# Performance work log

Measured on AMD Instinct MI355X. Metric: run time of the kernel, lower is better.

Reference implementation:

```python
import jax, jax.numpy as jnp
import numpy as np

N_HEADS = 16

def setup_inputs() -> dict:
    key = jax.random.key(0)
    qkv = jax.random.normal(key, (8, 3072, 1024), dtype=jnp.float32)
    return {"qkv": qkv}

def reference(qkv) -> jnp.ndarray:
    B, D, L = qkv.shape
    q, k, v = jnp.split(qkv, 3, axis=1)            # each [B, H*ch, L]
    ch = D // (3 * N_HEADS)
    scale = 1.0 / np.sqrt(np.sqrt(ch)).astype(np.float32)
    q = (q * scale).reshape(B * N_HEADS, ch, L)
    k = (k * scale).reshape(B * N_HEADS, ch, L)
    v = v.reshape(B * N_HEADS, ch, L)
    weight = jnp.einsum('bct,bcs->bts', q, k)       # [B*H, L, L]
    weight = jax.nn.softmax(weight, axis=-1)
    z = jnp.einsum('bts,bcs->bct', weight, v)       # [B*H, ch, L]
    return z.reshape(B, -1, L)
```

## Files before the change

kernel.cpp:

```cpp
#include <hip/hip_runtime.h>


typedef __attribute__((ext_vector_type(8))) _Float16 f16x8;
typedef __attribute__((ext_vector_type(4))) _Float16 f16x4;
typedef __attribute__((ext_vector_type(4))) float f32x4;

#define MAT_HALVES 8388608
#define WS_BYTES   33554432

#define ASYNC16(g, l) __builtin_amdgcn_global_load_lds(                    \
    (__attribute__((address_space(1))) void*)(void*)(g),                   \
    (__attribute__((address_space(3))) void*)(void*)(l), 16, 0, 0)

__global__ __launch_bounds__(256) void prepass_kv(
    const float* __restrict__ qkv, _Float16* __restrict__ ws) {
    __shared__ float ft[64][68];
    const int tid = threadIdx.x;
    const int bid = blockIdx.x;
    const int mat = bid >> 11;
    const int idx = bid & 2047;
    const int head = idx >> 4;
    const int blk  = idx & 15;
    const int b = head >> 4, h = head & 15;
    const float* src = qkv + (size_t)b * 3072 * 1024
                           + (size_t)((1 + mat) * 1024 + h * 64) * 1024;
    const int s0 = blk * 64;
    if (mat == 0) {
#pragma unroll
        for (int i = 0; i < 4; ++i) {
            const int c = i * 16 + (tid >> 4);
            const int s = (tid & 15) * 4;
            const float4 v = *(const float4*)(src + (size_t)c * 1024 + s0 + s);
            ft[s + 0][c] = v.x;
            ft[s + 1][c] = v.y;
            ft[s + 2][c] = v.z;
            ft[s + 3][c] = v.w;
        }
        __syncthreads();
        _Float16* dst = ws + (size_t)head * 65536 + (size_t)s0 * 64;
#pragma unroll
        for (int r = 0; r < 2; ++r) {
            const int g = r * 256 + tid;
            const int t = g >> 3, cb = g & 7;
            const float4 a = *(const float4*)&ft[t][cb * 8];
            const float4 bq = *(const float4*)&ft[t][cb * 8 + 4];
            f16x8 o = { (_Float16)a.x,  (_Float16)a.y,  (_Float16)a.z,  (_Float16)a.w,
                        (_Float16)bq.x, (_Float16)bq.y, (_Float16)bq.z, (_Float16)bq.w };
            *(f16x8*)(dst + (size_t)t * 64 + (size_t)(cb ^ (t & 7)) * 8) = o;
        }
    } else {
        _Float16* dst = ws + (size_t)MAT_HALVES + (size_t)head * 65536;
#pragma unroll
        for (int i = 0; i < 4; ++i) {
            const int c = i * 16 + (tid >> 4);
            const int s = (tid & 15) * 4;
            const float4 v = *(const float4*)(src + (size_t)c * 1024 + s0 + s);
            f16x4 o = { (_Float16)v.x, (_Float16)v.y, (_Float16)v.z, (_Float16)v.w };
            const int sb = s >> 3, pos = s & 7;
            *(f16x4*)(dst + (size_t)c * 1024 + s0 + (size_t)((sb ^ (c & 7)) * 8 + pos)) = o;
        }
    }
}

__launch_bounds__(512, 4)
__global__ void attn_kernel(const float* __restrict__ qkv,
                            const _Float16* __restrict__ ws,
                            float* __restrict__ out) {
    __shared__ __align__(16) union SM {
        _Float16 kv[2][8192];
        float ft[64][68];
    } sm;

    const int tid  = threadIdx.x;
    const int wv   = tid >> 6;
    const int lane = tid & 63;
    const int li   = lane & 15;
    const int quad = lane >> 4;

    const int bid  = blockIdx.x;
    const int head = (bid >> 5) * 8 + (bid & 7);
    const int tt   = (bid >> 3) & 3;
    const int t0   = tt * 256;

    const int b = head >> 4, h = head & 15;
    const float* qsrc = qkv + (size_t)b * 3072 * 1024 + (size_t)(h * 64) * 1024;
    const _Float16* kt = ws + (size_t)head * 65536;
    const _Float16* vh = ws + (size_t)MAT_HALVES + (size_t)head * 65536;

    const float qscale = 0.125f * 1.44269504f;
    f16x8 bqf[2][2];
    {
        const int ci = tid >> 4;
        const int tq = (tid & 15) * 4;
        for (int ct = 0; ct < 4; ++ct) {
#pragma unroll
            for (int i = 0; i < 2; ++i) {
                const int c = i * 32 + ci;
                const float4 v = *(const float4*)(qsrc + (size_t)c * 1024 + t0 + ct * 64 + tq);
                sm.ft[tq + 0][c] = v.x * qscale;
                sm.ft[tq + 1][c] = v.y * qscale;
                sm.ft[tq + 2][c] = v.z * qscale;
                sm.ft[tq + 3][c] = v.w * qscale;
            }
            __syncthreads();
            if ((wv >> 1) == ct) {
#pragma unroll
                for (int sub = 0; sub < 2; ++sub) {
                    const int tl = (wv & 1) * 32 + sub * 16 + li;
#pragma unroll
                    for (int kk = 0; kk < 2; ++kk) {
                        const int c0 = (kk * 4 + quad) * 8;
                        const float4 a  = *(const float4*)&sm.ft[tl][c0];
                        const float4 b2 = *(const float4*)&sm.ft[tl][c0 + 4];
                        bqf[sub][kk] = f16x8{ (_Float16)a.x,  (_Float16)a.y,
                                              (_Float16)a.z,  (_Float16)a.w,
                                              (_Float16)b2.x, (_Float16)b2.y,
                                              (_Float16)b2.z, (_Float16)b2.w };
                    }
                }
            }
            __syncthreads();
        }
    }

    ASYNC16(kt + (size_t)tid * 8, &sm.kv[0][tid * 8]);
    ASYNC16(vh + (size_t)(tid >> 3) * 1024 + (size_t)(tid & 7) * 8,
            &sm.kv[0][4096 + tid * 8]);

    f32x4 accz[2][4] = {};
    float psum[2] = {};

    for (int si = 0; si < 16; ++si) {
        __syncthreads();
        if (si < 15) {
            const int s0n = (si + 1) * 64;
            const int nb = (si + 1) & 1;
            ASYNC16(kt + (size_t)s0n * 64 + (size_t)tid * 8, &sm.kv[nb][tid * 8]);
            ASYNC16(vh + (size_t)(tid >> 3) * 1024 + s0n + (size_t)(tid & 7) * 8,
                    &sm.kv[nb][4096 + tid * 8]);
        }
        const _Float16* Kl = &sm.kv[si & 1][0];
        const _Float16* Vl = &sm.kv[si & 1][4096];

#pragma unroll
        for (int ns = 0; ns < 4; ++ns) {
            f16x8 ak[2];
#pragma unroll
            for (int kk = 0; kk < 2; ++kk) {
                const int cb = (kk * 4 + quad) ^ (li & 7);
                ak[kk] = *(const f16x8*)&Kl[(ns * 16 + li) * 64 + cb * 8];
            }
            f16x4 pk[2];
#pragma unroll
            for (int sub = 0; sub < 2; ++sub) {
                f32x4 st = {};
                st = __builtin_amdgcn_mfma_f32_16x16x32_f16(ak[0], bqf[sub][0], st, 0, 0, 0);
                st = __builtin_amdgcn_mfma_f32_16x16x32_f16(ak[1], bqf[sub][1], st, 0, 0, 0);
                const float p0 = __builtin_amdgcn_exp2f(st[0]);
                const float p1 = __builtin_amdgcn_exp2f(st[1]);
                const float p2 = __builtin_amdgcn_exp2f(st[2]);
                const float p3 = __builtin_amdgcn_exp2f(st[3]);
                psum[sub] += (p0 + p1) + (p2 + p3);
                pk[sub] = f16x4{ (_Float16)p0, (_Float16)p1,
                                 (_Float16)p2, (_Float16)p3 };
            }
            const int sb  = 2 * ns + (quad >> 1);
            const int pos = (quad & 1) * 4;
#pragma unroll
            for (int nc = 0; nc < 4; ++nc) {
                const int c = nc * 16 + li;
                f16x4 bv = *(const f16x4*)&Vl[c * 64 + ((sb ^ (c & 7)) << 3) + pos];
                accz[0][nc] = __builtin_amdgcn_mfma_f32_16x16x16f16(
                    pk[0], bv, accz[0][nc], 0, 0, 0);
                accz[1][nc] = __builtin_amdgcn_mfma_f32_16x16x16f16(
                    pk[1], bv, accz[1][nc], 0, 0, 0);
            }
        }
    }

    float rl[2][4];
#pragma unroll
    for (int sub = 0; sub < 2; ++sub) {
        float s = psum[sub];
        s += __shfl_xor(s, 16);
        s += __shfl_xor(s, 32);
#pragma unroll
        for (int r = 0; r < 4; ++r)
            rl[sub][r] = 1.0f / __shfl(s, quad * 4 + r);
    }

    float* obase = out + (size_t)b * 1024 * 1024
                       + (size_t)(h * 64) * 1024 + t0;
#pragma unroll
    for (int sub = 0; sub < 2; ++sub)
#pragma unroll
        for (int nc = 0; nc < 4; ++nc) {
            const int c = nc * 16 + li;
            const int t = wv * 32 + sub * 16 + quad * 4;
            f32x4 z = accz[sub][nc];
            float4 o = { z[0] * rl[sub][0], z[1] * rl[sub][1],
                         z[2] * rl[sub][2], z[3] * rl[sub][3] };
            *(float4*)(obase + (size_t)c * 1024 + t) = o;
        }
}

struct S1fb {
    _Float16 K[64][72];
    _Float16 V[64][72];
    _Float16 P[128][72];
};
union SMemFb {
    S1fb s1;
    float zt[64][132];
};

__launch_bounds__(256, 4)
__global__ void qkv_attn_fallback(const float* __restrict__ qkv,
                                  float* __restrict__ out) {
    constexpr int L = 1024;
    __shared__ SMemFb sm;
    const int tid  = threadIdx.x;
    const int wv   = tid >> 6;
    const int lane = tid & 63;
    const int li   = lane & 15;
    const int quad = lane >> 4;
    const int bid  = blockIdx.x;
    const int head = (bid >> 6) * 8 + (bid & 7);
    const int tt   = (bid >> 3) & 7;
    const int b = head >> 4;
    const int h = head & 15;
    const float* qbase = qkv + (size_t)b * 3072 * L + (size_t)(h * 64) * L;
    const float* kbase = qbase + (size_t)1024 * L;
    const float* vbase = qbase + (size_t)2048 * L;
    float*       obase = out + (size_t)b * 1024 * L + (size_t)(h * 64) * L;
    const int t0 = tt * 128;
#pragma unroll
    for (int i = 0; i < 4; ++i) {
        const int c = i * 16 + (tid >> 4);
        const int t = (tid & 15) * 8;
        const float4 qa = *(const float4*)(qbase + (size_t)c * L + t0 + t);
        const float4 qb = *(const float4*)(qbase + (size_t)c * L + t0 + t + 4);
        sm.s1.P[t + 0][c] = (_Float16)(qa.x * 0.125f);
        sm.s1.P[t + 1][c] = (_Float16)(qa.y * 0.125f);
        sm.s1.P[t + 2][c] = (_Float16)(qa.z * 0.125f);
        sm.s1.P[t + 3][c] = (_Float16)(qa.w * 0.125f);
        sm.s1.P[t + 4][c] = (_Float16)(qb.x * 0.125f);
        sm.s1.P[t + 5][c] = (_Float16)(qb.y * 0.125f);
        sm.s1.P[t + 6][c] = (_Float16)(qb.z * 0.125f);
        sm.s1.P[t + 7][c] = (_Float16)(qb.w * 0.125f);
    }
    __syncthreads();
    f16x8 aq0[2], aq1[2];
#pragma unroll
    for (int kk = 0; kk < 2; ++kk) {
        aq0[kk] = *(const f16x8*)&sm.s1.P[wv * 32 + li][kk * 32 + quad * 8];
        aq1[kk] = *(const f16x8*)&sm.s1.P[wv * 32 + 16 + li][kk * 32 + quad * 8];
    }
    f32x4 accz0[4] = {}, accz1[4] = {};
    float psum0[4] = {}, psum1[4] = {};
    float4 kreg[4], vreg[4];
#pragma unroll
    for (int i = 0; i < 4; ++i) {
        const int c = i * 16 + (tid >> 4);
        const int s = (tid & 15) * 4;
        kreg[i] = *(const float4*)(kbase + (size_t)c * L + s);
        vreg[i] = *(const float4*)(vbase + (size_t)c * L + s);
    }
    for (int si = 0; si < 16; ++si) {
        __syncthreads();
#pragma unroll
        for (int i = 0; i < 4; ++i) {
            const int c = i * 16 + (tid >> 4);
            const int s = (tid & 15) * 4;
            sm.s1.K[s + 0][c] = (_Float16)kreg[i].x;
            sm.s1.K[s + 1][c] = (_Float16)kreg[i].y;
            sm.s1.K[s + 2][c] = (_Float16)kreg[i].z;
            sm.s1.K[s + 3][c] = (_Float16)kreg[i].w;
            f16x4 pv = { (_Float16)vreg[i].x, (_Float16)vreg[i].y,
                         (_Float16)vreg[i].z, (_Float16)vreg[i].w };
            *(f16x4*)&sm.s1.V[c][s] = pv;
        }
        __syncthreads();
        if (si < 15) {
            const int s0n = (si + 1) * 64;
#pragma unroll
            for (int i = 0; i < 4; ++i) {
                const int c = i * 16 + (tid >> 4);
                const int s = (tid & 15) * 4;
                kreg[i] = *(const float4*)(kbase + (size_t)c * L + s0n + s);
                vreg[i] = *(const float4*)(vbase + (size_t)c * L + s0n + s);
            }
        }
#pragma unroll
        for (int nt = 0; nt < 4; ++nt) {
            f32x4 a0 = {}, a1 = {};
#pragma unroll
            for (int kk = 0; kk < 2; ++kk) {
                f16x8 bk = *(const f16x8*)&sm.s1.K[nt * 16 + li][kk * 32 + quad * 8];
                a0 = __builtin_amdgcn_mfma_f32_16x16x32_f16(aq0[kk], bk, a0, 0, 0, 0);
                a1 = __builtin_amdgcn_mfma_f32_16x16x32_f16(aq1[kk], bk, a1, 0, 0, 0);
            }
#pragma unroll
            for (int r = 0; r < 4; ++r) {
                const float p0 = __expf(a0[r]);
                const float p1 = __expf(a1[r]);
                psum0[r] += p0;
                psum1[r] += p1;
                sm.s1.P[wv * 32 + quad * 4 + r][nt * 16 + li] = (_Float16)p0;
                sm.s1.P[wv * 32 + 16 + quad * 4 + r][nt * 16 + li] = (_Float16)p1;
            }
        }
#pragma unroll
        for (int kk = 0; kk < 2; ++kk) {
            f16x8 ap0 = *(const f16x8*)&sm.s1.P[wv * 32 + li][kk * 32 + quad * 8];
            f16x8 ap1 = *(const f16x8*)&sm.s1.P[wv * 32 + 16 + li][kk * 32 + quad * 8];
#pragma unroll
            for (int nt = 0; nt < 4; ++nt) {
                f16x8 bv = *(const f16x8*)&sm.s1.V[nt * 16 + li][kk * 32 + quad * 8];
                accz0[nt] = __builtin_amdgcn_mfma_f32_16x16x32_f16(ap0, bv, accz0[nt], 0, 0, 0);
                accz1[nt] = __builtin_amdgcn_mfma_f32_16x16x32_f16(ap1, bv, accz1[nt], 0, 0, 0);
            }
        }
    }
    float rl0[4], rl1[4];
#pragma unroll
    for (int r = 0; r < 4; ++r) {
        float s0 = psum0[r], s1 = psum1[r];
        s0 += __shfl_xor(s0, 1); s0 += __shfl_xor(s0, 2);
        s0 += __shfl_xor(s0, 4); s0 += __shfl_xor(s0, 8);
        s1 += __shfl_xor(s1, 1); s1 += __shfl_xor(s1, 2);
        s1 += __shfl_xor(s1, 4); s1 += __shfl_xor(s1, 8);
        rl0[r] = 1.0f / s0;
        rl1[r] = 1.0f / s1;
    }
    __syncthreads();
#pragma unroll
    for (int nt = 0; nt < 4; ++nt)
#pragma unroll
        for (int r = 0; r < 4; ++r) {
            sm.zt[nt * 16 + li][wv * 32 + quad * 4 + r]      = accz0[nt][r] * rl0[r];
            sm.zt[nt * 16 + li][wv * 32 + 16 + quad * 4 + r] = accz1[nt][r] * rl1[r];
        }
    __syncthreads();
#pragma unroll
    for (int i = 0; i < 8; ++i) {
        const int c = i * 8 + (tid >> 5);
        const int t = (tid & 31) * 4;
        float4 o = { sm.zt[c][t], sm.zt[c][t + 1],
                     sm.zt[c][t + 2], sm.zt[c][t + 3] };
        *(float4*)(obase + (size_t)c * L + t0 + t) = o;
    }
}

extern "C" void kernel_launch(void* const* d_in, const int* in_sizes, int n_in,
                              void* d_out, int out_size, void* d_ws, size_t ws_size,
                              hipStream_t stream) {
    const float* qkv = (const float*)d_in[0];
    float* out = (float*)d_out;
    if (ws_size >= (size_t)WS_BYTES) {
        _Float16* ws = (_Float16*)d_ws;
        prepass_kv<<<4096, 256, 0, stream>>>(qkv, ws);
        attn_kernel<<<512, 512, 0, stream>>>(qkv, ws, out);
    } else {
        qkv_attn_fallback<<<1024, 256, 0, stream>>>(qkv, out);
    }
}
```

Baseline: 195.9 us.

## Deepen K/V LDS pipeline to four buffers and overlap prologue loads with Q staging

Grows the K/V shared-memory ring from two to four 16KB stages. The first two tiles are prefetched before Q is processed, and each barrier step now covers two tiles, which halves the number of __syncthreads in the main loop. All Q global loads are also hoisted into registers before the LDS transpose, so their latencies overlap. The cost is 64KB of LDS per block instead of 32KB plus more live registers, which may reduce how many blocks fit on each CU.

```diff
diff --git a/kernel.cpp b/kernel.cpp
--- a/kernel.cpp
+++ b/kernel.cpp
@@ -67,7 +67,7 @@
                             const _Float16* __restrict__ ws,
                             float* __restrict__ out) {
     __shared__ __align__(16) union SM {
-        _Float16 kv[2][8192];
+        _Float16 kv[4][8192];
         float ft[64][68];
     } sm;
 
@@ -87,93 +87,111 @@
     const _Float16* kt = ws + (size_t)head * 65536;
     const _Float16* vh = ws + (size_t)MAT_HALVES + (size_t)head * 65536;
 
+#pragma unroll
+    for (int u = 0; u < 2; ++u) {
+        const int s0 = u * 64;
+        ASYNC16(kt + (size_t)s0 * 64 + (size_t)tid * 8, &sm.kv[2 + u][tid * 8]);
+        ASYNC16(vh + (size_t)(tid >> 3) * 1024 + s0 + (size_t)(tid & 7) * 8,
+                &sm.kv[2 + u][4096 + tid * 8]);
+    }
+
     const float qscale = 0.125f * 1.44269504f;
+    const int ci = tid >> 4;
+    const int tq = (tid & 15) * 4;
+    float4 qv[4][2];
+#pragma unroll
+    for (int ct = 0; ct < 4; ++ct)
+#pragma unroll
+        for (int i = 0; i < 2; ++i) {
+            const int c = i * 32 + ci;
+            qv[ct][i] = *(const float4*)(qsrc + (size_t)c * 1024 + t0 + ct * 64 + tq);
+        }
     f16x8 bqf[2][2];
-    {
-        const int ci = tid >> 4;
-        const int tq = (tid & 15) * 4;
-        for (int ct = 0; ct < 4; ++ct) {
-#pragma unroll
-            for (int i = 0; i < 2; ++i) {
-                const int c = i * 32 + ci;
-                const float4 v = *(const float4*)(qsrc + (size_t)c * 1024 + t0 + ct * 64 + tq);
-                sm.ft[tq + 0][c] = v.x * qscale;
-                sm.ft[tq + 1][c] = v.y * qscale;
-                sm.ft[tq + 2][c] = v.z * qscale;
-                sm.ft[tq + 3][c] = v.w * qscale;
-            }
-            __syncthreads();
-            if ((wv >> 1) == ct) {
-#pragma unroll
-                for (int sub = 0; sub < 2; ++sub) {
-                    const int tl = (wv & 1) * 32 + sub * 16 + li;
-#pragma unroll
-                    for (int kk = 0; kk < 2; ++kk) {
-                        const int c0 = (kk * 4 + quad) * 8;
-                        const float4 a  = *(const float4*)&sm.ft[tl][c0];
-                        const float4 b2 = *(const float4*)&sm.ft[tl][c0 + 4];
-                        bqf[sub][kk] = f16x8{ (_Float16)a.x,  (_Float16)a.y,
-                                              (_Float16)a.z,  (_Float16)a.w,
-                                              (_Float16)b2.x, (_Float16)b2.y,
-                                              (_Float16)b2.z, (_Float16)b2.w };
-                    }
+#pragma unroll
+    for (int ct = 0; ct < 4; ++ct) {
+#pragma unroll
+        for (int i = 0; i < 2; ++i) {
+            const int c = i * 32 + ci;
+            sm.ft[tq + 0][c] = qv[ct][i].x * qscale;
+            sm.ft[tq + 1][c] = qv[ct][i].y * qscale;
+            sm.ft[tq + 2][c] = qv[ct][i].z * qscale;
+            sm.ft[tq + 3][c] = qv[ct][i].w * qscale;
+        }
+        __syncthreads();
+        if ((wv >> 1) == ct) {
+#pragma unroll
+            for (int sub = 0; sub < 2; ++sub) {
+                const int tl = (wv & 1) * 32 + sub * 16 + li;
+#pragma unroll
+                for (int kk = 0; kk < 2; ++kk) {
+                    const int c0 = (kk * 4 + quad) * 8;
+                    const float4 a  = *(const float4*)&sm.ft[tl][c0];
+                    const float4 b2 = *(const float4*)&sm.ft[tl][c0 + 4];
+                    bqf[sub][kk] = f16x8{ (_Float16)a.x,  (_Float16)a.y,
+                                          (_Float16)a.z,  (_Float16)a.w,
+                                          (_Float16)b2.x, (_Float16)b2.y,
+                                          (_Float16)b2.z, (_Float16)b2.w };
                 }
             }
-            __syncthreads();
-        }
-    }
-
-    ASYNC16(kt + (size_t)tid * 8, &sm.kv[0][tid * 8]);
-    ASYNC16(vh + (size_t)(tid >> 3) * 1024 + (size_t)(tid & 7) * 8,
-            &sm.kv[0][4096 + tid * 8]);
+        }
+        __syncthreads();
+    }
 
     f32x4 accz[2][4] = {};
     float psum[2] = {};
 
-    for (int si = 0; si < 16; ++si) {
-        __syncthreads();
-        if (si < 15) {
-            const int s0n = (si + 1) * 64;
-            const int nb = (si + 1) & 1;
-            ASYNC16(kt + (size_t)s0n * 64 + (size_t)tid * 8, &sm.kv[nb][tid * 8]);
-            ASYNC16(vh + (size_t)(tid >> 3) * 1024 + s0n + (size_t)(tid & 7) * 8,
-                    &sm.kv[nb][4096 + tid * 8]);
-        }
-        const _Float16* Kl = &sm.kv[si & 1][0];
-        const _Float16* Vl = &sm.kv[si & 1][4096];
-
-#pragma unroll
-        for (int ns = 0; ns < 4; ++ns) {
-            f16x8 ak[2];
-#pragma unroll
-            for (int kk = 0; kk < 2; ++kk) {
-                const int cb = (kk * 4 + quad) ^ (li & 7);
-                ak[kk] = *(const f16x8*)&Kl[(ns * 16 + li) * 64 + cb * 8];
-            }
-            f16x4 pk[2];
-#pragma unroll
-            for (int sub = 0; sub < 2; ++sub) {
-                f32x4 st = {};
-                st = __builtin_amdgcn_mfma_f32_16x16x32_f16(ak[0], bqf[sub][0], st, 0, 0, 0);
-                st = __builtin_amdgcn_mfma_f32_16x16x32_f16(ak[1], bqf[sub][1], st, 0, 0, 0);
-                const float p0 = __builtin_amdgcn_exp2f(st[0]);
-                const float p1 = __builtin_amdgcn_exp2f(st[1]);
-                const float p2 = __builtin_amdgcn_exp2f(st[2]);
-                const float p3 = __builtin_amdgcn_exp2f(st[3]);
-                psum[sub] += (p0 + p1) + (p2 + p3);
-                pk[sub] = f16x4{ (_Float16)p0, (_Float16)p1,
-                                 (_Float16)p2, (_Float16)p3 };
-            }
-            const int sb  = 2 * ns + (quad >> 1);
-            const int pos = (quad & 1) * 4;
-#pragma unroll
-            for (int nc = 0; nc < 4; ++nc) {
-                const int c = nc * 16 + li;
-                f16x4 bv = *(const f16x4*)&Vl[c * 64 + ((sb ^ (c & 7)) << 3) + pos];
-                accz[0][nc] = __builtin_amdgcn_mfma_f32_16x16x16f16(
-                    pk[0], bv, accz[0][nc], 0, 0, 0);
-                accz[1][nc] = __builtin_amdgcn_mfma_f32_16x16x16f16(
-                    pk[1], bv, accz[1][nc], 0, 0, 0);
+    for (int p = 0; p < 8; ++p) {
+        __syncthreads();
+        if (p < 7) {
+#pragma unroll
+            for (int u = 0; u < 2; ++u) {
+                const int sn  = 2 * p + 2 + u;
+                const int s0n = sn * 64;
+                const int nb  = (sn + 2) & 3;
+                ASYNC16(kt + (size_t)s0n * 64 + (size_t)tid * 8, &sm.kv[nb][tid * 8]);
+                ASYNC16(vh + (size_t)(tid >> 3) * 1024 + s0n + (size_t)(tid & 7) * 8,
+                        &sm.kv[nb][4096 + tid * 8]);
+            }
+        }
+#pragma unroll
+        for (int u = 0; u < 2; ++u) {
+            const int si = 2 * p + u;
+            const _Float16* Kl = &sm.kv[(si + 2) & 3][0];
+            const _Float16* Vl = &sm.kv[(si + 2) & 3][4096];
+
+#pragma unroll
+            for (int ns = 0; ns < 4; ++ns) {
+                f16x8 ak[2];
+#pragma unroll
+                for (int kk = 0; kk < 2; ++kk) {
+                    const int cb = (kk * 4 + quad) ^ (li & 7);
+                    ak[kk] = *(const f16x8*)&Kl[(ns * 16 + li) * 64 + cb * 8];
+                }
+                f16x4 pk[2];
+#pragma unroll
+                for (int sub = 0; sub < 2; ++sub) {
+                    f32x4 st = {};
+                    st = __builtin_amdgcn_mfma_f32_16x16x32_f16(ak[0], bqf[sub][0], st, 0, 0, 0);
+                    st = __builtin_amdgcn_mfma_f32_16x16x32_f16(ak[1], bqf[sub][1], st, 0, 0, 0);
+                    const float p0 = __builtin_amdgcn_exp2f(st[0]);
+                    const float p1 = __builtin_amdgcn_exp2f(st[1]);
+                    const float p2 = __builtin_amdgcn_exp2f(st[2]);
+                    const float p3 = __builtin_amdgcn_exp2f(st[3]);
+                    psum[sub] += (p0 + p1) + (p2 + p3);
+                    pk[sub] = f16x4{ (_Float16)p0, (_Float16)p1,
+                                     (_Float16)p2, (_Float16)p3 };
+                }
+                const int sb  = 2 * ns + (quad >> 1);
+                const int pos = (quad & 1) * 4;
+#pragma unroll
+                for (int nc = 0; nc < 4; ++nc) {
+                    const int c = nc * 16 + li;
+                    f16x4 bv = *(const f16x4*)&Vl[c * 64 + ((sb ^ (c & 7)) << 3) + pos];
+                    accz[0][nc] = __builtin_amdgcn_mfma_f32_16x16x16f16(
+                        pk[0], bv, accz[0][nc], 0, 0, 0);
+                    accz[1][nc] = __builtin_amdgcn_mfma_f32_16x16x16f16(
+                        pk[1], bv, accz[1][nc], 0, 0, 0);
+                }
             }
         }
     }
```

Measured after the change: 229.9 us. +17.4%, slower.

## Halve attention block to 4 waves, each computing 64 query rows

Applied to the files above, without the earlier changes.

The attention kernel now launches 256 threads instead of 512. Each wave processes 64 query rows (4 sub-tiles) instead of 32, so every K/V fragment read from LDS feeds twice as many MFMAs. The K/V shared buffers are no longer unioned with the Q transpose buffer, which lets the first two K/V tiles be prefetched asynchronously before the Q load. s_setprio is raised around the MFMA loop. The cost is more accumulator registers per thread and fewer waves per block to hide latency, with occupancy bounded at 2 blocks.

```diff
diff --git a/kernel.cpp b/kernel.cpp
--- a/kernel.cpp
+++ b/kernel.cpp
@@ -62,14 +62,12 @@
     }
 }
 
-__launch_bounds__(512, 4)
+__launch_bounds__(256, 2)
 __global__ void attn_kernel(const float* __restrict__ qkv,
                             const _Float16* __restrict__ ws,
                             float* __restrict__ out) {
-    __shared__ __align__(16) union SM {
-        _Float16 kv[2][8192];
-        float ft[64][68];
-    } sm;
+    __shared__ __align__(16) _Float16 kv[2][8192];
+    __shared__ __align__(16) float ft[64][68];
 
     const int tid  = threadIdx.x;
     const int wv   = tid >> 6;
@@ -87,61 +85,71 @@
     const _Float16* kt = ws + (size_t)head * 65536;
     const _Float16* vh = ws + (size_t)MAT_HALVES + (size_t)head * 65536;
 
+#pragma unroll
+    for (int u = 0; u < 2; ++u) {
+        const int s0 = u * 64;
+#pragma unroll
+        for (int j = 0; j < 2; ++j) {
+            const int g = j * 256 + tid;
+            ASYNC16(kt + (size_t)s0 * 64 + (size_t)g * 8, &kv[u][g * 8]);
+            ASYNC16(vh + (size_t)(g >> 3) * 1024 + s0 + (size_t)(g & 7) * 8,
+                    &kv[u][4096 + g * 8]);
+        }
+    }
+
     const float qscale = 0.125f * 1.44269504f;
-    f16x8 bqf[2][2];
-    {
-        const int ci = tid >> 4;
-        const int tq = (tid & 15) * 4;
-        for (int ct = 0; ct < 4; ++ct) {
-#pragma unroll
-            for (int i = 0; i < 2; ++i) {
-                const int c = i * 32 + ci;
-                const float4 v = *(const float4*)(qsrc + (size_t)c * 1024 + t0 + ct * 64 + tq);
-                sm.ft[tq + 0][c] = v.x * qscale;
-                sm.ft[tq + 1][c] = v.y * qscale;
-                sm.ft[tq + 2][c] = v.z * qscale;
-                sm.ft[tq + 3][c] = v.w * qscale;
-            }
-            __syncthreads();
-            if ((wv >> 1) == ct) {
-#pragma unroll
-                for (int sub = 0; sub < 2; ++sub) {
-                    const int tl = (wv & 1) * 32 + sub * 16 + li;
-#pragma unroll
-                    for (int kk = 0; kk < 2; ++kk) {
-                        const int c0 = (kk * 4 + quad) * 8;
-                        const float4 a  = *(const float4*)&sm.ft[tl][c0];
-                        const float4 b2 = *(const float4*)&sm.ft[tl][c0 + 4];
-                        bqf[sub][kk] = f16x8{ (_Float16)a.x,  (_Float16)a.y,
-                                              (_Float16)a.z,  (_Float16)a.w,
-                                              (_Float16)b2.x, (_Float16)b2.y,
-                                              (_Float16)b2.z, (_Float16)b2.w };
-                    }
+    f16x8 bqf[4][2];
+    for (int ct = 0; ct < 4; ++ct) {
+#pragma unroll
+        for (int i = 0; i < 4; ++i) {
+            const int c = i * 16 + (tid >> 4);
+            const int t = (tid & 15) * 4;
+            const float4 v = *(const float4*)(qsrc + (size_t)c * 1024 + t0 + ct * 64 + t);
+            ft[t + 0][c] = v.x * qscale;
+            ft[t + 1][c] = v.y * qscale;
+            ft[t + 2][c] = v.z * qscale;
+            ft[t + 3][c] = v.w * qscale;
+        }
+        __syncthreads();
+        if (wv == ct) {
+#pragma unroll
+            for (int sub = 0; sub < 4; ++sub) {
+                const int tl = sub * 16 + li;
+#pragma unroll
+                for (int kk = 0; kk < 2; ++kk) {
+                    const int c0 = (kk * 4 + quad) * 8;
+                    const float4 a  = *(const float4*)&ft[tl][c0];
+                    const float4 b2 = *(const float4*)&ft[tl][c0 + 4];
+                    bqf[sub][kk] = f16x8{ (_Float16)a.x,  (_Float16)a.y,
+                                          (_Float16)a.z,  (_Float16)a.w,
+                                          (_Float16)b2.x, (_Float16)b2.y,
+                                          (_Float16)b2.z, (_Float16)b2.w };
                 }
             }
-            __syncthreads();
-        }
-    }
-
-    ASYNC16(kt + (size_t)tid * 8, &sm.kv[0][tid * 8]);
-    ASYNC16(vh + (size_t)(tid >> 3) * 1024 + (size_t)(tid & 7) * 8,
-            &sm.kv[0][4096 + tid * 8]);
-
-    f32x4 accz[2][4] = {};
-    float psum[2] = {};
+        }
+        __syncthreads();
+    }
+
+    f32x4 accz[4][4] = {};
+    float psum[4] = {};
 
     for (int si = 0; si < 16; ++si) {
         __syncthreads();
         if (si < 15) {
             const int s0n = (si + 1) * 64;
             const int nb = (si + 1) & 1;
-            ASYNC16(kt + (size_t)s0n * 64 + (size_t)tid * 8, &sm.kv[nb][tid * 8]);
-            ASYNC16(vh + (size_t)(tid >> 3) * 1024 + s0n + (size_t)(tid & 7) * 8,
-                    &sm.kv[nb][4096 + tid * 8]);
-        }
-        const _Float16* Kl = &sm.kv[si & 1][0];
-        const _Float16* Vl = &sm.kv[si & 1][4096];
-
+#pragma unroll
+            for (int j = 0; j < 2; ++j) {
+                const int g = j * 256 + tid;
+                ASYNC16(kt + (size_t)s0n * 64 + (size_t)g * 8, &kv[nb][g * 8]);
+                ASYNC16(vh + (size_t)(g >> 3) * 1024 + s0n + (size_t)(g & 7) * 8,
+                        &kv[nb][4096 + g * 8]);
+            }
+        }
+        const _Float16* Kl = &kv[si & 1][0];
+        const _Float16* Vl = &kv[si & 1][4096];
+
+        __builtin_amdgcn_s_setprio(1);
 #pragma unroll
         for (int ns = 0; ns < 4; ++ns) {
             f16x8 ak[2];
@@ -150,9 +158,9 @@
                 const int cb = (kk * 4 + quad) ^ (li & 7);
                 ak[kk] = *(const f16x8*)&Kl[(ns * 16 + li) * 64 + cb * 8];
             }
-            f16x4 pk[2];
-#pragma unroll
-            for (int sub = 0; sub < 2; ++sub) {
+            f16x4 pk[4];
+#pragma unroll
+            for (int sub = 0; sub < 4; ++sub) {
                 f32x4 st = {};
                 st = __builtin_amdgcn_mfma_f32_16x16x32_f16(ak[0], bqf[sub][0], st, 0, 0, 0);
                 st = __builtin_amdgcn_mfma_f32_16x16x32_f16(ak[1], bqf[sub][1], st, 0, 0, 0);
@@ -170,17 +178,18 @@
             for (int nc = 0; nc < 4; ++nc) {
                 const int c = nc * 16 + li;
                 f16x4 bv = *(const f16x4*)&Vl[c * 64 + ((sb ^ (c & 7)) << 3) + pos];
-                accz[0][nc] = __builtin_amdgcn_mfma_f32_16x16x16f16(
-                    pk[0], bv, accz[0][nc], 0, 0, 0);
-                accz[1][nc] = __builtin_amdgcn_mfma_f32_16x16x16f16(
-                    pk[1], bv, accz[1][nc], 0, 0, 0);
-            }
-        }
-    }
-
-    float rl[2][4];
-#pragma unroll
-    for (int sub = 0; sub < 2; ++sub) {
+#pragma unroll
+                for (int sub = 0; sub < 4; ++sub)
+                    accz[sub][nc] = __builtin_amdgcn_mfma_f32_16x16x16f16(
+                        pk[sub], bv, accz[sub][nc], 0, 0, 0);
+            }
+        }
+        __builtin_amdgcn_s_setprio(0);
+    }
+
+    float rl[4][4];
+#pragma unroll
+    for (int sub = 0; sub < 4; ++sub) {
         float s = psum[sub];
         s += __shfl_xor(s, 16);
         s += __shfl_xor(s, 32);
@@ -192,11 +201,11 @@
     float* obase = out + (size_t)b * 1024 * 1024
                        + (size_t)(h * 64) * 1024 + t0;
 #pragma unroll
-    for (int sub = 0; sub < 2; ++sub)
+    for (int sub = 0; sub < 4; ++sub)
 #pragma unroll
         for (int nc = 0; nc < 4; ++nc) {
             const int c = nc * 16 + li;
-            const int t = wv * 32 + sub * 16 + quad * 4;
+            const int t = wv * 64 + sub * 16 + quad * 4;
             f32x4 z = accz[sub][nc];
             float4 o = { z[0] * rl[sub][0], z[1] * rl[sub][1],
                          z[2] * rl[sub][2], z[3] * rl[sub][3] };
@@ -360,7 +369,7 @@
     if (ws_size >= (size_t)WS_BYTES) {
         _Float16* ws = (_Float16*)d_ws;
         prepass_kv<<<4096, 256, 0, stream>>>(qkv, ws);
-        attn_kernel<<<512, 512, 0, stream>>>(qkv, ws, out);
+        attn_kernel<<<512, 256, 0, stream>>>(qkv, ws, out);
     } else {
         qkv_attn_fallback<<<1024, 256, 0, stream>>>(qkv, out);
     }
```

Result: no change. 193.3 us (-1.3%).

## Load V directly from global into registers and prefetch K before Q setup

Applied to the files above, without the earlier changes.

V tiles are no longer staged through double-buffered LDS. Each thread loads its MFMA B-operand fragments of V straight from global memory into registers at the start of each step, and the prepass stops swizzling V. K's first two tiles are prefetched asynchronously before the Q transpose, which now uses its own LDS buffer instead of a union, and setprio is raised around the MFMA loop. The occupancy hint drops from 4 to 2. This saves LDS traffic and space for V and overlaps the K load with Q setup, at the cost of strided, less coalesced global loads of V and more register pressure.

```diff
diff --git a/kernel.cpp b/kernel.cpp
--- a/kernel.cpp
+++ b/kernel.cpp
@@ -56,20 +56,17 @@
             const int s = (tid & 15) * 4;
             const float4 v = *(const float4*)(src + (size_t)c * 1024 + s0 + s);
             f16x4 o = { (_Float16)v.x, (_Float16)v.y, (_Float16)v.z, (_Float16)v.w };
-            const int sb = s >> 3, pos = s & 7;
-            *(f16x4*)(dst + (size_t)c * 1024 + s0 + (size_t)((sb ^ (c & 7)) * 8 + pos)) = o;
+            *(f16x4*)(dst + (size_t)c * 1024 + s0 + s) = o;
         }
     }
 }
 
-__launch_bounds__(512, 4)
+__launch_bounds__(512, 2)
 __global__ void attn_kernel(const float* __restrict__ qkv,
                             const _Float16* __restrict__ ws,
                             float* __restrict__ out) {
-    __shared__ __align__(16) union SM {
-        _Float16 kv[2][8192];
-        float ft[64][68];
-    } sm;
+    __shared__ __align__(16) _Float16 kv[2][4096];
+    __shared__ __align__(16) float ft[64][68];
 
     const int tid  = threadIdx.x;
     const int wv   = tid >> 6;
@@ -86,6 +83,9 @@
     const float* qsrc = qkv + (size_t)b * 3072 * 1024 + (size_t)(h * 64) * 1024;
     const _Float16* kt = ws + (size_t)head * 65536;
     const _Float16* vh = ws + (size_t)MAT_HALVES + (size_t)head * 65536;
+
+    ASYNC16(kt + (size_t)tid * 8, &kv[0][tid * 8]);
+    ASYNC16(kt + (size_t)4096 + (size_t)tid * 8, &kv[1][tid * 8]);
 
     const float qscale = 0.125f * 1.44269504f;
     f16x8 bqf[2][2];
@@ -97,10 +97,10 @@
             for (int i = 0; i < 2; ++i) {
                 const int c = i * 32 + ci;
                 const float4 v = *(const float4*)(qsrc + (size_t)c * 1024 + t0 + ct * 64 + tq);
-                sm.ft[tq + 0][c] = v.x * qscale;
-                sm.ft[tq + 1][c] = v.y * qscale;
-                sm.ft[tq + 2][c] = v.z * qscale;
-                sm.ft[tq + 3][c] = v.w * qscale;
+                ft[tq + 0][c] = v.x * qscale;
+                ft[tq + 1][c] = v.y * qscale;
+                ft[tq + 2][c] = v.z * qscale;
+                ft[tq + 3][c] = v.w * qscale;
             }
             __syncthreads();
             if ((wv >> 1) == ct) {
@@ -110,8 +110,8 @@
 #pragma unroll
                     for (int kk = 0; kk < 2; ++kk) {
                         const int c0 = (kk * 4 + quad) * 8;
-                        const float4 a  = *(const float4*)&sm.ft[tl][c0];
-                        const float4 b2 = *(const float4*)&sm.ft[tl][c0 + 4];
+                        const float4 a  = *(const float4*)&ft[tl][c0];
+                        const float4 b2 = *(const float4*)&ft[tl][c0 + 4];
                         bqf[sub][kk] = f16x8{ (_Float16)a.x,  (_Float16)a.y,
                                               (_Float16)a.z,  (_Float16)a.w,
                                               (_Float16)b2.x, (_Float16)b2.y,
@@ -123,10 +123,6 @@
         }
     }
 
-    ASYNC16(kt + (size_t)tid * 8, &sm.kv[0][tid * 8]);
-    ASYNC16(vh + (size_t)(tid >> 3) * 1024 + (size_t)(tid & 7) * 8,
-            &sm.kv[0][4096 + tid * 8]);
-
     f32x4 accz[2][4] = {};
     float psum[2] = {};
 
@@ -134,14 +130,22 @@
         __syncthreads();
         if (si < 15) {
             const int s0n = (si + 1) * 64;
-            const int nb = (si + 1) & 1;
-            ASYNC16(kt + (size_t)s0n * 64 + (size_t)tid * 8, &sm.kv[nb][tid * 8]);
-            ASYNC16(vh + (size_t)(tid >> 3) * 1024 + s0n + (size_t)(tid & 7) * 8,
-                    &sm.kv[nb][4096 + tid * 8]);
-        }
-        const _Float16* Kl = &sm.kv[si & 1][0];
-        const _Float16* Vl = &sm.kv[si & 1][4096];
-
+            ASYNC16(kt + (size_t)s0n * 64 + (size_t)tid * 8,
+                    &kv[(si + 1) & 1][tid * 8]);
+        }
+        const _Float16* Kl = &kv[si & 1][0];
+        const _Float16* Vg = vh + si * 64;
+
+        f16x4 vr[4][4];
+#pragma unroll
+        for (int ns = 0; ns < 4; ++ns)
+#pragma unroll
+            for (int nc = 0; nc < 4; ++nc) {
+                const int c = nc * 16 + li;
+                vr[ns][nc] = *(const f16x4*)(Vg + (size_t)c * 1024 + ns * 16 + quad * 4);
+            }
+
+        __builtin_amdgcn_s_setprio(1);
 #pragma unroll
         for (int ns = 0; ns < 4; ++ns) {
             f16x8 ak[2];
@@ -164,18 +168,15 @@
                 pk[sub] = f16x4{ (_Float16)p0, (_Float16)p1,
                                  (_Float16)p2, (_Float16)p3 };
             }
-            const int sb  = 2 * ns + (quad >> 1);
-            const int pos = (quad & 1) * 4;
 #pragma unroll
             for (int nc = 0; nc < 4; ++nc) {
-                const int c = nc * 16 + li;
-                f16x4 bv = *(const f16x4*)&Vl[c * 64 + ((sb ^ (c & 7)) << 3) + pos];
                 accz[0][nc] = __builtin_amdgcn_mfma_f32_16x16x16f16(
-                    pk[0], bv, accz[0][nc], 0, 0, 0);
+                    pk[0], vr[ns][nc], accz[0][nc], 0, 0, 0);
                 accz[1][nc] = __builtin_amdgcn_mfma_f32_16x16x16f16(
-                    pk[1], bv, accz[1][nc], 0, 0, 0);
-            }
-        }
+                    pk[1], vr[ns][nc], accz[1][nc], 0, 0, 0);
+            }
+        }
+        __builtin_amdgcn_s_setprio(0);
     }
 
     float rl[2][4];
```

New measurement: 278.6 us. +42.2%, slower.
